# Kernel tuning notes

Hardware: AMD Instinct MI355X
Metric: run time of the kernel (lower is better)

## Reference

```python
import jax, jax.numpy as jnp
import numpy as np


def setup_inputs() -> dict:
    key = jax.random.key(0)
    k1, k2, k3, k4 = jax.random.split(key, 4)
    HIDDEN = 1024
    L1_CAP = 4096
    L2_CAP = 16384
    B = 4096
    return {
        "query": jax.random.normal(k1, (B, HIDDEN), dtype=jnp.float32),
        "W": jax.random.normal(k2, (HIDDEN, HIDDEN), dtype=jnp.float32) * (1.0 / np.sqrt(HIDDEN)),
        "l1": jax.random.normal(k3, (L1_CAP, HIDDEN), dtype=jnp.float32),
        "l2": jax.random.normal(k4, (L2_CAP, HIDDEN), dtype=jnp.float32),
        "l1_mask": jnp.ones((L1_CAP,), dtype=bool),
        "l2_mask": jnp.ones((L2_CAP,), dtype=bool),
        "top_k": 16,
    }


def reference(query, W, l1, l2, l1_mask, l2_mask, top_k):
    # score_proj: Linear(hidden, hidden, bias=False) -> q @ W.T
    q_proj = query @ W.T                      # [B, H]
    mem = jnp.concatenate([l1, l2], axis=0)   # [M, H]
    mask = jnp.concatenate([l1_mask, l2_mask], axis=0)  # [M]
    # masked scoring
    scores = q_proj @ mem.T                   # [B, M]
    scores = jnp.where(mask[None, :], scores, -jnp.inf)
    # top-k selection + softmax weighting (masks are all True -> k == top_k)
    vals, idx = jax.lax.top_k(scores, top_k)  # [B, K]
    soft = jax.nn.softmax(vals, axis=-1)      # [B, K]
    # gathered memory is detached in the original (mem[idx].detach())
    gathered = jax.lax.stop_gradient(mem)[idx]  # [B, K, H]
    gathered = gathered * soft[..., None]
    return gathered
```

## Files before the change

kernel.cpp:

```cpp
#include <hip/hip_runtime.h>


#define HIDDEN 1024
#define BQ     4096
#define TOPK   16
#define MTOT   20480

typedef __attribute__((ext_vector_type(8)))  short s8v;
typedef __attribute__((ext_vector_type(4)))  float f4v;
typedef __attribute__((ext_vector_type(16))) float f16v;
typedef __attribute__((ext_vector_type(4)))  int   i4v;
typedef __attribute__((ext_vector_type(8)))  int   i8v;

#define WAITVM(N) asm volatile("s_waitcnt vmcnt(" #N ")" ::: "memory")

static __device__ __forceinline__ unsigned short f32_to_bf16_rne(float f) {
  unsigned u = __float_as_uint(f);
  unsigned r = 0x7FFFu + ((u >> 16) & 1u);
  return (unsigned short)((u + r) >> 16);
}
static __device__ __forceinline__ float bf16_to_f32(unsigned short h) {
  return __uint_as_float(((unsigned)h) << 16);
}

__global__ __launch_bounds__(256) void hm_cvt_split(
    const float* __restrict__ in, unsigned short* __restrict__ hi,
    unsigned short* __restrict__ lo, int n4) {
  int i = blockIdx.x * 256 + threadIdx.x;
  if (i >= n4) return;
  float4 x = ((const float4*)in)[i];
  ushort4 h, l;
  h.x = f32_to_bf16_rne(x.x); l.x = f32_to_bf16_rne(x.x - bf16_to_f32(h.x));
  h.y = f32_to_bf16_rne(x.y); l.y = f32_to_bf16_rne(x.y - bf16_to_f32(h.y));
  h.z = f32_to_bf16_rne(x.z); l.z = f32_to_bf16_rne(x.z - bf16_to_f32(h.z));
  h.w = f32_to_bf16_rne(x.w); l.w = f32_to_bf16_rne(x.w - bf16_to_f32(h.w));
  ((ushort4*)hi)[i] = h;
  ((ushort4*)lo)[i] = l;
}

__global__ __launch_bounds__(256) void hm_cvt_fp8(
    const float* __restrict__ in, unsigned char* __restrict__ out8, int n8) {
  int i = blockIdx.x * 256 + threadIdx.x;
  if (i >= n8) return;
  const float4* p = (const float4*)in + (size_t)i * 2;
  float4 x = p[0], y = p[1];
  int u0 = __builtin_amdgcn_cvt_pk_fp8_f32(x.x, x.y, 0, false);
  u0     = __builtin_amdgcn_cvt_pk_fp8_f32(x.z, x.w, u0, true);
  int u1 = __builtin_amdgcn_cvt_pk_fp8_f32(y.x, y.y, 0, false);
  u1     = __builtin_amdgcn_cvt_pk_fp8_f32(y.z, y.w, u1, true);
  uint2 o; o.x = (unsigned)u0; o.y = (unsigned)u1;
  ((uint2*)out8)[i] = o;
}

__global__ __launch_bounds__(256) void hm_cvt_mem_fp8(
    const float* __restrict__ l1, const float* __restrict__ l2,
    unsigned char* __restrict__ out8) {
  int i = blockIdx.x * 256 + threadIdx.x;
  int row = i >> 7, colg = i & 127;
  const float* src = (row < 4096) ? (l1 + (size_t)row * HIDDEN + colg * 8)
                                  : (l2 + (size_t)(row - 4096) * HIDDEN + colg * 8);
  float4 x = ((const float4*)src)[0], y = ((const float4*)src)[1];
  int u0 = __builtin_amdgcn_cvt_pk_fp8_f32(x.x, x.y, 0, false);
  u0     = __builtin_amdgcn_cvt_pk_fp8_f32(x.z, x.w, u0, true);
  int u1 = __builtin_amdgcn_cvt_pk_fp8_f32(y.x, y.y, 0, false);
  u1     = __builtin_amdgcn_cvt_pk_fp8_f32(y.z, y.w, u1, true);
  uint2 o; o.x = (unsigned)u0; o.y = (unsigned)u1;
  ((uint2*)out8)[i] = o;
}

__global__ __launch_bounds__(256) void hm_gemm_split3(
    const unsigned short* __restrict__ Ahi, const unsigned short* __restrict__ Alo,
    const unsigned short* __restrict__ Bhi, const unsigned short* __restrict__ Blo,
    float* __restrict__ Cf, int N, int K) {
  __shared__ unsigned short lds[2][16384];
  const int tid = threadIdx.x, lane = tid & 63, w = tid >> 6;
  const int m0 = blockIdx.x * 128, n0 = blockIdx.y * 128;
  const int wr = (w >> 1) * 64, wc = (w & 1) * 64;
  f4v acc[4][4] = {};
  const unsigned short* plane = (w == 0) ? Ahi : (w == 1) ? Alo : (w == 2) ? Bhi : Blo;
  const int gbase = (w < 2) ? m0 : n0;
  const int kg = lane >> 4, r16 = lane & 15;
  const int NT = K / 32;

  auto STAGE = [&](int cur, int t) {
#pragma unroll
    for (int is = 0; is < 8; ++is) {
      int slot = is * 64 + lane;
      int row = slot >> 2, kgs = slot & 3;
      const unsigned short* gp = plane + (size_t)(gbase + row) * K + (t * 32 + kgs * 8);
      unsigned short* lp = &lds[cur][(w * 512 + is * 64) * 8];
      __builtin_amdgcn_global_load_lds(
          (const __attribute__((address_space(1))) unsigned int*)gp,
          (__attribute__((address_space(3))) unsigned int*)lp, 16, 0, 0);
    }
  };

  STAGE(0, 0);
  __syncthreads();
  for (int t = 0; t < NT; ++t) {
    int cur = t & 1;
    if (t + 1 < NT) STAGE(cur ^ 1, t + 1);

    s8v ah[4], al[4], bh[4], bl[4];
#pragma unroll
    for (int mi = 0; mi < 4; ++mi) {
      int ro = wr + mi * 16 + r16;
      ah[mi] = *(const s8v*)&lds[cur][(0 * 512 + ro * 4 + kg) * 8];
      al[mi] = *(const s8v*)&lds[cur][(1 * 512 + ro * 4 + kg) * 8];
    }
#pragma unroll
    for (int ni = 0; ni < 4; ++ni) {
      int ro = wc + ni * 16 + r16;
      bh[ni] = *(const s8v*)&lds[cur][(2 * 512 + ro * 4 + kg) * 8];
      bl[ni] = *(const s8v*)&lds[cur][(3 * 512 + ro * 4 + kg) * 8];
    }
#pragma unroll
    for (int mi = 0; mi < 4; ++mi)
#pragma unroll
      for (int ni = 0; ni < 4; ++ni) {
        acc[mi][ni] = __builtin_amdgcn_mfma_f32_16x16x32_bf16(ah[mi], bh[ni], acc[mi][ni], 0, 0, 0);
        acc[mi][ni] = __builtin_amdgcn_mfma_f32_16x16x32_bf16(ah[mi], bl[ni], acc[mi][ni], 0, 0, 0);
        acc[mi][ni] = __builtin_amdgcn_mfma_f32_16x16x32_bf16(al[mi], bh[ni], acc[mi][ni], 0, 0, 0);
      }
    __syncthreads();
  }
  const int cr = (lane >> 4) * 4, cc = lane & 15;
#pragma unroll
  for (int mi = 0; mi < 4; ++mi)
#pragma unroll
    for (int ni = 0; ni < 4; ++ni)
#pragma unroll
      for (int j = 0; j < 4; ++j) {
        int R = m0 + wr + mi * 16 + cr + j;
        int Cc = n0 + wc + ni * 16 + cc;
        Cf[(size_t)R * N + Cc] = acc[mi][ni][j];
      }
}

__global__ __launch_bounds__(256, 2) void hm_gemm_fp8(
    const unsigned char* __restrict__ A8, const unsigned char* __restrict__ B8,
    unsigned short* __restrict__ Cbf, int N, int K) {
  __shared__ __align__(16) char smem[73728];
  const int tid = threadIdx.x, lane = tid & 63, w = tid >> 6;
  const int m0 = blockIdx.x * 128, n0 = blockIdx.y * 256;
  const int wr = (w >> 1) * 64;
  const int wc = (w & 1) * 128;
  const int l31 = lane & 31, lh = lane >> 5;
  const int sc = 0x7F7F7F7F;
  const int NT = K / 64;

  f16v acc[2][4] = {};

  auto STAGE = [&](int cur, int t) {
    char* bA = smem + cur * 24576;
    char* bB = bA + 8192;
    int k0 = t * 64;
#pragma unroll
    for (int r0 = 0; r0 < 128; r0 += 64) {
      const unsigned char* gA = A8 + (size_t)(m0 + r0 + lane) * K + (k0 + w * 16);
      __builtin_amdgcn_global_load_lds(
          (const __attribute__((address_space(1))) unsigned int*)gA,
          (__attribute__((address_space(3))) unsigned int*)(bA + (w * 128 + r0) * 16),
          16, 0, 0);
    }
#pragma unroll
    for (int r0 = 0; r0 < 256; r0 += 64) {
      const unsigned char* gB = B8 + (size_t)(n0 + r0 + lane) * K + (k0 + w * 16);
      __builtin_amdgcn_global_load_lds(
          (const __attribute__((address_space(1))) unsigned int*)gB,
          (__attribute__((address_space(3))) unsigned int*)(bB + (w * 256 + r0) * 16),
          16, 0, 0);
    }
  };

  STAGE(0, 0);
  STAGE(1, 1);
  for (int t = 0; t < NT; ++t) {
    __builtin_amdgcn_s_barrier();
    if (t + 2 < NT)      { STAGE((t + 2) % 3, t + 2); WAITVM(12); }
    else if (t + 1 < NT) { WAITVM(6); }
    else                 { WAITVM(0); }
    __builtin_amdgcn_s_barrier();

    char* bA = smem + (t % 3) * 24576;
    char* bB = bA + 8192;
    i8v a[2], b[4];
#pragma unroll
    for (int mi = 0; mi < 2; ++mi) {
      int ch = (lh * 2) * 128 + wr + mi * 32 + l31;
      i4v lo = *(const i4v*)(bA + ch * 16);
      i4v hi = *(const i4v*)(bA + ch * 16 + 2048);
      i8v v; v[0]=lo[0]; v[1]=lo[1]; v[2]=lo[2]; v[3]=lo[3];
             v[4]=hi[0]; v[5]=hi[1]; v[6]=hi[2]; v[7]=hi[3];
      a[mi] = v;
    }
#pragma unroll
    for (int ni = 0; ni < 4; ++ni) {
      int ch = (lh * 2) * 256 + wc + ni * 32 + l31;
      i4v lo = *(const i4v*)(bB + ch * 16);
      i4v hi = *(const i4v*)(bB + ch * 16 + 4096);
      i8v v; v[0]=lo[0]; v[1]=lo[1]; v[2]=lo[2]; v[3]=lo[3];
             v[4]=hi[0]; v[5]=hi[1]; v[6]=hi[2]; v[7]=hi[3];
      b[ni] = v;
    }
    __builtin_amdgcn_s_setprio(1);
#pragma unroll
    for (int mi = 0; mi < 2; ++mi)
#pragma unroll
      for (int ni = 0; ni < 4; ++ni)
        acc[mi][ni] = __builtin_amdgcn_mfma_scale_f32_32x32x64_f8f6f4(
            a[mi], b[ni], acc[mi][ni], 0, 0, 0, sc, 0, sc);
    __builtin_amdgcn_s_setprio(0);
  }

  __syncthreads();
  short* ldsC = (short*)smem;
#pragma unroll
  for (int mi = 0; mi < 2; ++mi)
#pragma unroll
    for (int ni = 0; ni < 4; ++ni)
#pragma unroll
      for (int r = 0; r < 16; ++r) {
        int row = wr + mi * 32 + ((r & 3) + 8 * (r >> 2) + 4 * lh);
        int col = wc + ni * 32 + l31;
        ldsC[row * 256 + col] = (short)f32_to_bf16_rne(acc[mi][ni][r]);
      }
  __syncthreads();
#pragma unroll
  for (int it = 0; it < 16; ++it) {
    int idx = it * 256 + tid;
    int row = idx >> 5, c8 = idx & 31;
    uint4 v = *(const uint4*)(ldsC + row * 256 + c8 * 8);
    *(uint4*)(Cbf + (size_t)(m0 + row) * N + n0 + c8 * 8) = v;
  }
}

__global__ __launch_bounds__(256) void hm_topk(
    const unsigned short* __restrict__ scores, int* __restrict__ stIdx) {
  int tid = threadIdx.x, lane = tid & 63, w = tid >> 6;
  int b = blockIdx.x * 4 + w;
  const uint4* row = (const uint4*)(scores + (size_t)b * MTOT);

  unsigned q[8];
#pragma unroll
  for (int i = 0; i < 8; ++i) q[i] = 0;

  auto push = [&](unsigned p) {
    if (p > q[7]) {
      q[7] = p;
#pragma unroll
      for (int i = 7; i > 0; --i) {
        unsigned hi = q[i - 1] > q[i] ? q[i - 1] : q[i];
        unsigned lo = q[i - 1] > q[i] ? q[i] : q[i - 1];
        q[i - 1] = hi; q[i] = lo;
      }
    }
  };

  for (int it = 0; it < MTOT / 512; ++it) {
    uint4 pk = row[it * 64 + lane];
    unsigned base = (it * 64 + lane) * 8;
    unsigned u4[4] = {pk.x, pk.y, pk.z, pk.w};
#pragma unroll
    for (int j = 0; j < 4; ++j) {
      unsigned v0 = u4[j] & 0xffffu, v1 = u4[j] >> 16;
      unsigned k0 = v0 ^ ((v0 >> 15) ? 0xFFFFu : 0x8000u);
      unsigned k1 = v1 ^ ((v1 >> 15) ? 0xFFFFu : 0x8000u);
      push((k0 << 16) | (base + 2 * j));
      push((k1 << 16) | (base + 2 * j + 1));
    }
  }

  unsigned keep = 0;
#pragma unroll
  for (int r = 0; r < TOPK; ++r) {
    unsigned m = q[0];
#pragma unroll
    for (int mk = 1; mk < 64; mk <<= 1) {
      unsigned o = (unsigned)__shfl_xor((int)m, mk);
      m = m > o ? m : o;
    }
    if (q[0] == m) {
#pragma unroll
      for (int i = 0; i < 7; ++i) q[i] = q[i + 1];
      q[7] = 0;
    }
    if (lane == r) keep = m;
  }
  if (lane < TOPK) stIdx[b * TOPK + lane] = (int)(keep & 0xffffu);
}

__global__ __launch_bounds__(256) void hm_refine_gather(
    const float* __restrict__ qp, const int* __restrict__ stIdx,
    const float* __restrict__ l1, const float* __restrict__ l2,
    float* __restrict__ out) {
  __shared__ float vals[TOPK], wts[TOPK], red[TOPK][4], ssum[1];
  __shared__ int rankOf[TOPK], sidx[TOPK];
  int b = blockIdx.x, tid = threadIdx.x;
  int lane = tid & 63, w = tid >> 6;
  if (tid < TOPK) sidx[tid] = stIdx[b * TOPK + tid];
  float4 q4 = ((const float4*)(qp + (size_t)b * HIDDEN))[tid];
  __syncthreads();

  float4 m4[TOPK];
  float p[TOPK];
#pragma unroll
  for (int k = 0; k < TOPK; ++k) {
    int idx = sidx[k];
    const float4* mr = (idx < 4096) ? (const float4*)(l1 + (size_t)idx * HIDDEN)
                                    : (const float4*)(l2 + (size_t)(idx - 4096) * HIDDEN);
    m4[k] = mr[tid];
    p[k] = q4.x * m4[k].x + q4.y * m4[k].y + q4.z * m4[k].z + q4.w * m4[k].w;
  }
#pragma unroll
  for (int k = 0; k < TOPK; ++k)
#pragma unroll
    for (int mask = 1; mask < 64; mask <<= 1) p[k] += __shfl_xor(p[k], mask);
  if (lane == 0)
#pragma unroll
    for (int k = 0; k < TOPK; ++k) red[k][w] = p[k];
  __syncthreads();
  if (tid < TOPK) vals[tid] = red[tid][0] + red[tid][1] + red[tid][2] + red[tid][3];
  __syncthreads();
  if (tid < TOPK) {
    float vt = vals[tid];
    int it = sidx[tid], r = 0;
    float m = vals[0];
#pragma unroll
    for (int j = 0; j < TOPK; ++j) {
      float vj = vals[j];
      m = fmaxf(m, vj);
      r += (vj > vt || (vj == vt && sidx[j] < it)) ? 1 : 0;
    }
    rankOf[tid] = r;
    wts[tid] = expf(vt - m);
  }
  __syncthreads();
  if (tid == 0) {
    float s = 0.f;
#pragma unroll
    for (int j = 0; j < TOPK; ++j) s += wts[j];
    ssum[0] = s;
  }
  __syncthreads();
  float inv = 1.0f / ssum[0];
#pragma unroll
  for (int k = 0; k < TOPK; ++k) {
    float wt = wts[k] * inv;
    int r = rankOf[k];
    float4 x = m4[k];
    x.x *= wt; x.y *= wt; x.z *= wt; x.w *= wt;
    ((float4*)out)[((size_t)b * TOPK + r) * 256 + tid] = x;
  }
}

extern "C" void kernel_launch(void* const* d_in, const int* in_sizes, int n_in,
                              void* d_out, int out_size, void* d_ws, size_t ws_size,
                              hipStream_t stream) {
  const float* query = (const float*)d_in[0];
  const float* W     = (const float*)d_in[1];
  const float* l1    = (const float*)d_in[2];
  const float* l2    = (const float*)d_in[3];
  float* out = (float*)d_out;

  const size_t MiB = 1024 * 1024;
  char* ws = (char*)d_ws;
  unsigned short* qh  = (unsigned short*)(ws + 0);
  unsigned short* ql  = (unsigned short*)(ws + 8 * MiB);
  unsigned short* wh  = (unsigned short*)(ws + 16 * MiB);
  unsigned short* wl  = (unsigned short*)(ws + 18 * MiB);
  float*          qpf = (float*)(ws + 20 * MiB);
  unsigned char*  qp8 = (unsigned char*)(ws + 0);
  int*            stIdx = (int*)(ws + 36 * MiB);

  unsigned short* scores = (unsigned short*)d_out;
  unsigned char*  mem8   = (unsigned char*)d_out + 200 * MiB;

  hm_cvt_split<<<dim3(BQ * HIDDEN / 1024), dim3(256), 0, stream>>>(query, qh, ql, BQ * HIDDEN / 4);
  hm_cvt_split<<<dim3(HIDDEN * HIDDEN / 1024), dim3(256), 0, stream>>>(W, wh, wl, HIDDEN * HIDDEN / 4);
  hm_gemm_split3<<<dim3(BQ / 128, HIDDEN / 128), dim3(256), 0, stream>>>(
      qh, ql, wh, wl, qpf, HIDDEN, HIDDEN);
  hm_cvt_fp8<<<dim3(BQ * HIDDEN / 2048), dim3(256), 0, stream>>>(qpf, qp8, BQ * HIDDEN / 8);
  hm_cvt_mem_fp8<<<dim3(MTOT * HIDDEN / 2048), dim3(256), 0, stream>>>(l1, l2, mem8);

  hm_gemm_fp8<<<dim3(BQ / 128, MTOT / 256), dim3(256), 0, stream>>>(
      qp8, mem8, scores, MTOT, HIDDEN);
  hm_topk<<<dim3(BQ / 4), dim3(256), 0, stream>>>(scores, stIdx);
  hm_refine_gather<<<dim3(BQ), dim3(256), 0, stream>>>(qpf, stIdx, l1, l2, out);
}
```

Baseline: 343.4 us.

## Restructure FP8 scoring GEMM: smaller tiles, A in registers, swizzled grid, fused conversions

The FP8 score GEMM moves from 128x256 tiles with triple-buffered LDS for A and B to 128x128 tiles. A fragments are loaded straight from global memory into registers, and only B is double-buffered in LDS. A 1D grid with a block-index swizzle is added for L2 locality, and launch bounds now allow 3 blocks per CU. The two bf16 split-conversion launches are merged into one kernel. The aim is higher occupancy and less LDS traffic, at the cost of more global A reads per output and an extra barrier per K step.

After: 445.7 us. 1.3x slower.

```diff
diff --git a/kernel.cpp b/kernel.cpp
--- a/kernel.cpp
+++ b/kernel.cpp
@@ -23,19 +23,25 @@
   return __uint_as_float(((unsigned)h) << 16);
 }
 
-__global__ __launch_bounds__(256) void hm_cvt_split(
-    const float* __restrict__ in, unsigned short* __restrict__ hi,
-    unsigned short* __restrict__ lo, int n4) {
+__global__ __launch_bounds__(256) void hm_cvt_split2(
+    const float* __restrict__ q, const float* __restrict__ W,
+    unsigned short* __restrict__ qh, unsigned short* __restrict__ ql,
+    unsigned short* __restrict__ wh, unsigned short* __restrict__ wl) {
+  const int NQ = BQ * HIDDEN / 4;
   int i = blockIdx.x * 256 + threadIdx.x;
-  if (i >= n4) return;
-  float4 x = ((const float4*)in)[i];
+  const float* in;
+  unsigned short *ho, *lo;
+  int j;
+  if (i < NQ) { in = q; j = i;      ho = qh; lo = ql; }
+  else        { in = W; j = i - NQ; ho = wh; lo = wl; }
+  float4 x = ((const float4*)in)[j];
   ushort4 h, l;
   h.x = f32_to_bf16_rne(x.x); l.x = f32_to_bf16_rne(x.x - bf16_to_f32(h.x));
   h.y = f32_to_bf16_rne(x.y); l.y = f32_to_bf16_rne(x.y - bf16_to_f32(h.y));
   h.z = f32_to_bf16_rne(x.z); l.z = f32_to_bf16_rne(x.z - bf16_to_f32(h.z));
   h.w = f32_to_bf16_rne(x.w); l.w = f32_to_bf16_rne(x.w - bf16_to_f32(h.w));
-  ((ushort4*)hi)[i] = h;
-  ((ushort4*)lo)[i] = l;
+  ((ushort4*)ho)[j] = h;
+  ((ushort4*)lo)[j] = l;
 }
 
 __global__ __launch_bounds__(256) void hm_cvt_fp8(
@@ -137,80 +143,97 @@
       }
 }
 
-__global__ __launch_bounds__(256, 2) void hm_gemm_fp8(
+__global__ __launch_bounds__(256, 3) void hm_gemm_fp8(
     const unsigned char* __restrict__ A8, const unsigned char* __restrict__ B8,
     unsigned short* __restrict__ Cbf, int N, int K) {
-  __shared__ __align__(16) char smem[73728];
+  __shared__ __align__(16) char smem[32768];
   const int tid = threadIdx.x, lane = tid & 63, w = tid >> 6;
-  const int m0 = blockIdx.x * 128, n0 = blockIdx.y * 256;
-  const int wr = (w >> 1) * 64;
-  const int wc = (w & 1) * 128;
+  const int bid = blockIdx.x;
+  const int swz = (bid & 7) * 640 + (bid >> 3);
+  const int m0 = (swz & 31) * 128;
+  const int n0 = (swz >> 5) * 128;
+  const int wr = (w >> 1) * 64, wc = (w & 1) * 64;
   const int l31 = lane & 31, lh = lane >> 5;
   const int sc = 0x7F7F7F7F;
-  const int NT = K / 64;
-
-  f16v acc[2][4] = {};
-
-  auto STAGE = [&](int cur, int t) {
-    char* bA = smem + cur * 24576;
-    char* bB = bA + 8192;
-    int k0 = t * 64;
-#pragma unroll
-    for (int r0 = 0; r0 < 128; r0 += 64) {
-      const unsigned char* gA = A8 + (size_t)(m0 + r0 + lane) * K + (k0 + w * 16);
+  const int NT = 16;
+
+  f16v acc[2][2] = {};
+
+  const unsigned char* pa0 = A8 + (size_t)(m0 + wr + l31) * K + lh * 32;
+  const unsigned char* pa1 = A8 + (size_t)(m0 + wr + 32 + l31) * K + lh * 32;
+
+  auto STAGE_B = [&](int buf, int t) {
+#pragma unroll
+    for (int p = 0; p < 2; ++p) {
+      int slot = p * 256 + tid;
+      int kc = slot >> 7, row = slot & 127;
+      const unsigned char* g = B8 + (size_t)(n0 + row) * K + t * 64 + kc * 16;
       __builtin_amdgcn_global_load_lds(
-          (const __attribute__((address_space(1))) unsigned int*)gA,
-          (__attribute__((address_space(3))) unsigned int*)(bA + (w * 128 + r0) * 16),
+          (const __attribute__((address_space(1))) unsigned int*)g,
+          (__attribute__((address_space(3))) unsigned int*)(smem + buf * 8192 + slot * 16),
           16, 0, 0);
     }
-#pragma unroll
-    for (int r0 = 0; r0 < 256; r0 += 64) {
-      const unsigned char* gB = B8 + (size_t)(n0 + r0 + lane) * K + (k0 + w * 16);
-      __builtin_amdgcn_global_load_lds(
-          (const __attribute__((address_space(1))) unsigned int*)gB,
-          (__attribute__((address_space(3))) unsigned int*)(bB + (w * 256 + r0) * 16),
-          16, 0, 0);
-    }
   };
 
-  STAGE(0, 0);
-  STAGE(1, 1);
+  i4v a0lo0, a0hi0, a0lo1, a0hi1;
+  i4v a1lo0, a1hi0, a1lo1, a1hi1;
+
+  a0lo0 = *(const i4v*)(pa0 + 0);  a0hi0 = *(const i4v*)(pa0 + 16);
+  a0lo1 = *(const i4v*)(pa1 + 0);  a0hi1 = *(const i4v*)(pa1 + 16);
+  STAGE_B(0, 0);
+  a1lo0 = *(const i4v*)(pa0 + 64); a1hi0 = *(const i4v*)(pa0 + 80);
+  a1lo1 = *(const i4v*)(pa1 + 64); a1hi1 = *(const i4v*)(pa1 + 80);
+  STAGE_B(1, 1);
+
+#pragma unroll
   for (int t = 0; t < NT; ++t) {
+    if (t < NT - 1) { WAITVM(6); } else { WAITVM(0); }
     __builtin_amdgcn_s_barrier();
-    if (t + 2 < NT)      { STAGE((t + 2) % 3, t + 2); WAITVM(12); }
-    else if (t + 1 < NT) { WAITVM(6); }
-    else                 { WAITVM(0); }
-    __builtin_amdgcn_s_barrier();
-
-    char* bA = smem + (t % 3) * 24576;
-    char* bB = bA + 8192;
-    i8v a[2], b[4];
-#pragma unroll
-    for (int mi = 0; mi < 2; ++mi) {
-      int ch = (lh * 2) * 128 + wr + mi * 32 + l31;
-      i4v lo = *(const i4v*)(bA + ch * 16);
-      i4v hi = *(const i4v*)(bA + ch * 16 + 2048);
-      i8v v; v[0]=lo[0]; v[1]=lo[1]; v[2]=lo[2]; v[3]=lo[3];
-             v[4]=hi[0]; v[5]=hi[1]; v[6]=hi[2]; v[7]=hi[3];
-      a[mi] = v;
-    }
-#pragma unroll
-    for (int ni = 0; ni < 4; ++ni) {
-      int ch = (lh * 2) * 256 + wc + ni * 32 + l31;
+
+    const char* bB = smem + (t & 1) * 8192;
+    i8v a[2], b[2];
+    if ((t & 1) == 0) {
+      a[0][0]=a0lo0[0]; a[0][1]=a0lo0[1]; a[0][2]=a0lo0[2]; a[0][3]=a0lo0[3];
+      a[0][4]=a0hi0[0]; a[0][5]=a0hi0[1]; a[0][6]=a0hi0[2]; a[0][7]=a0hi0[3];
+      a[1][0]=a0lo1[0]; a[1][1]=a0lo1[1]; a[1][2]=a0lo1[2]; a[1][3]=a0lo1[3];
+      a[1][4]=a0hi1[0]; a[1][5]=a0hi1[1]; a[1][6]=a0hi1[2]; a[1][7]=a0hi1[3];
+    } else {
+      a[0][0]=a1lo0[0]; a[0][1]=a1lo0[1]; a[0][2]=a1lo0[2]; a[0][3]=a1lo0[3];
+      a[0][4]=a1hi0[0]; a[0][5]=a1hi0[1]; a[0][6]=a1hi0[2]; a[0][7]=a1hi0[3];
+      a[1][0]=a1lo1[0]; a[1][1]=a1lo1[1]; a[1][2]=a1lo1[2]; a[1][3]=a1lo1[3];
+      a[1][4]=a1hi1[0]; a[1][5]=a1hi1[1]; a[1][6]=a1hi1[2]; a[1][7]=a1hi1[3];
+    }
+#pragma unroll
+    for (int ni = 0; ni < 2; ++ni) {
+      int ch = (lh * 2) * 128 + wc + ni * 32 + l31;
       i4v lo = *(const i4v*)(bB + ch * 16);
-      i4v hi = *(const i4v*)(bB + ch * 16 + 4096);
-      i8v v; v[0]=lo[0]; v[1]=lo[1]; v[2]=lo[2]; v[3]=lo[3];
-             v[4]=hi[0]; v[5]=hi[1]; v[6]=hi[2]; v[7]=hi[3];
-      b[ni] = v;
+      i4v hi = *(const i4v*)(bB + ch * 16 + 2048);
+      b[ni][0]=lo[0]; b[ni][1]=lo[1]; b[ni][2]=lo[2]; b[ni][3]=lo[3];
+      b[ni][4]=hi[0]; b[ni][5]=hi[1]; b[ni][6]=hi[2]; b[ni][7]=hi[3];
     }
     __builtin_amdgcn_s_setprio(1);
 #pragma unroll
     for (int mi = 0; mi < 2; ++mi)
 #pragma unroll
-      for (int ni = 0; ni < 4; ++ni)
+      for (int ni = 0; ni < 2; ++ni)
         acc[mi][ni] = __builtin_amdgcn_mfma_scale_f32_32x32x64_f8f6f4(
             a[mi], b[ni], acc[mi][ni], 0, 0, 0, sc, 0, sc);
     __builtin_amdgcn_s_setprio(0);
+
+    asm volatile("s_waitcnt lgkmcnt(0)" ::: "memory");
+    __builtin_amdgcn_sched_barrier(0);
+    __builtin_amdgcn_s_barrier();
+    if (t + 2 < NT) {
+      int tt = t + 2;
+      if ((tt & 1) == 0) {
+        a0lo0 = *(const i4v*)(pa0 + tt * 64);      a0hi0 = *(const i4v*)(pa0 + tt * 64 + 16);
+        a0lo1 = *(const i4v*)(pa1 + tt * 64);      a0hi1 = *(const i4v*)(pa1 + tt * 64 + 16);
+      } else {
+        a1lo0 = *(const i4v*)(pa0 + tt * 64);      a1hi0 = *(const i4v*)(pa0 + tt * 64 + 16);
+        a1lo1 = *(const i4v*)(pa1 + tt * 64);      a1hi1 = *(const i4v*)(pa1 + tt * 64 + 16);
+      }
+      STAGE_B(tt & 1, tt);
+    }
   }
 
   __syncthreads();
@@ -218,20 +241,20 @@
 #pragma unroll
   for (int mi = 0; mi < 2; ++mi)
 #pragma unroll
-    for (int ni = 0; ni < 4; ++ni)
+    for (int ni = 0; ni < 2; ++ni)
 #pragma unroll
       for (int r = 0; r < 16; ++r) {
         int row = wr + mi * 32 + ((r & 3) + 8 * (r >> 2) + 4 * lh);
         int col = wc + ni * 32 + l31;
-        ldsC[row * 256 + col] = (short)f32_to_bf16_rne(acc[mi][ni][r]);
+        ldsC[row * 128 + col] = (short)f32_to_bf16_rne(acc[mi][ni][r]);
       }
   __syncthreads();
 #pragma unroll
-  for (int it = 0; it < 16; ++it) {
+  for (int it = 0; it < 8; ++it) {
     int idx = it * 256 + tid;
-    int row = idx >> 5, c8 = idx & 31;
-    uint4 v = *(const uint4*)(ldsC + row * 256 + c8 * 8);
-    *(uint4*)(Cbf + (size_t)(m0 + row) * N + n0 + c8 * 8) = v;
+    int row = idx >> 4, c16 = idx & 15;
+    uint4 v = *(const uint4*)(ldsC + row * 128 + c16 * 8);
+    *(uint4*)(Cbf + (size_t)(m0 + row) * N + n0 + c16 * 8) = v;
   }
 }
 
@@ -376,14 +399,14 @@
   unsigned short* scores = (unsigned short*)d_out;
   unsigned char*  mem8   = (unsigned char*)d_out + 200 * MiB;
 
-  hm_cvt_split<<<dim3(BQ * HIDDEN / 1024), dim3(256), 0, stream>>>(query, qh, ql, BQ * HIDDEN / 4);
-  hm_cvt_split<<<dim3(HIDDEN * HIDDEN / 1024), dim3(256), 0, stream>>>(W, wh, wl, HIDDEN * HIDDEN / 4);
+  hm_cvt_split2<<<dim3((BQ * HIDDEN + HIDDEN * HIDDEN) / 1024), dim3(256), 0, stream>>>(
+      query, W, qh, ql, wh, wl);
   hm_gemm_split3<<<dim3(BQ / 128, HIDDEN / 128), dim3(256), 0, stream>>>(
       qh, ql, wh, wl, qpf, HIDDEN, HIDDEN);
   hm_cvt_fp8<<<dim3(BQ * HIDDEN / 2048), dim3(256), 0, stream>>>(qpf, qp8, BQ * HIDDEN / 8);
   hm_cvt_mem_fp8<<<dim3(MTOT * HIDDEN / 2048), dim3(256), 0, stream>>>(l1, l2, mem8);
 
-  hm_gemm_fp8<<<dim3(BQ / 128, MTOT / 256), dim3(256), 0, stream>>>(
+  hm_gemm_fp8<<<dim3((BQ / 128) * (MTOT / 128)), dim3(256), 0, stream>>>(
       qp8, mem8, scores, MTOT, HIDDEN);
   hm_topk<<<dim3(BQ / 4), dim3(256), 0, stream>>>(scores, stIdx);
   hm_refine_gather<<<dim3(BQ), dim3(256), 0, stream>>>(qpf, stIdx, l1, l2, out);
```
